# Kernel optimization log

Measured on AMD Instinct MI355X. Metric: run time of the kernel, lower is better.

Reference implementation:

```python
import jax, jax.numpy as jnp
import numpy as np

B, C, P = 16, 512, 4096


def setup_inputs() -> dict:
    key = jax.random.key(0)
    ks = jax.random.split(key, 7)
    s = 1.0 / np.sqrt(C)  # torch Conv1d default init scale
    return {
        "x": jax.random.normal(ks[0], (B, C, P), dtype=jnp.float32),
        "Wq": jax.random.uniform(ks[1], (C, C), jnp.float32, -s, s),
        "bq": jax.random.uniform(ks[2], (C,), jnp.float32, -s, s),
        "Wk": jax.random.uniform(ks[3], (C, C), jnp.float32, -s, s),
        "bk": jax.random.uniform(ks[4], (C,), jnp.float32, -s, s),
        "Wv": jax.random.uniform(ks[5], (C, C), jnp.float32, -s, s),
        "bv": jax.random.uniform(ks[6], (C,), jnp.float32, -s, s),
    }


def reference(x, Wq, bq, Wk, bk, Wv, bv):
    # 1x1 Conv1d == channel-mixing GEMM: out[b,o,p] = sum_i W[o,i] x[b,i,p] + b[o]
    q = jnp.einsum('oi,bip->bop', Wq, x) + bq[None, :, None]   # [B,C,P]
    k = jnp.einsum('oi,bip->bop', Wk, x) + bk[None, :, None]   # [B,C,P]
    v = jnp.einsum('oi,bip->bop', Wv, x) + bv[None, :, None]   # [B,C,P]
    energy = jnp.einsum('bcp,bdp->bcd', q, k)                  # [B,C,C] (unscaled)
    attn = jax.nn.softmax(energy, axis=-1)
    out = jnp.einsum('bcd,bdp->bcp', attn, v)                  # [B,C,P]
    return out
```

## Files before the change

### kernel.cpp

```cpp
#include <hip/hip_runtime.h>
#include <hip/hip_bf16.h>

#define CD 512
#define PD 4096
#define BD 16
#define CAUG 640
#define KW 576

typedef __bf16 bf16x8 __attribute__((ext_vector_type(8)));
typedef float f32x4 __attribute__((ext_vector_type(4)));
typedef unsigned short u16x8 __attribute__((ext_vector_type(8)));
typedef unsigned short u16x4 __attribute__((ext_vector_type(4)));

__device__ __forceinline__ unsigned short f2bf(float f) {
  unsigned u = __builtin_bit_cast(unsigned, f);
  u += 0x7FFFu + ((u >> 16) & 1u);
  return (unsigned short)(u >> 16);
}
__device__ __forceinline__ float bf2f(unsigned short h) {
  unsigned u = ((unsigned)h) << 16;
  return __builtin_bit_cast(float, u);
}

__global__ void convert_w2(const float* __restrict__ Wq, const float* __restrict__ bq,
                           const float* __restrict__ Wk, const float* __restrict__ bk,
                           const float* __restrict__ Wv,
                           unsigned short* __restrict__ Wqh, unsigned short* __restrict__ Wql,
                           unsigned short* __restrict__ Wkh, unsigned short* __restrict__ Wkl,
                           unsigned short* __restrict__ Wvh) {
  int i = blockIdx.x * 256 + threadIdx.x;
  if (i >= CD * KW) return;
  int o = i / KW, j = i - o * KW;
  float q = j < CD ? Wq[o * CD + j] : (j == CD ? bq[o] : 0.f);
  float k = j < CD ? Wk[o * CD + j] : (j == CD ? bk[o] : 0.f);
  unsigned short qh = f2bf(q), kh = f2bf(k);
  Wqh[i] = qh; Wql[i] = f2bf(q - bf2f(qh));
  Wkh[i] = kh; Wkl[i] = f2bf(k - bf2f(kh));
  if (j < CD) Wvh[o * CD + j] = f2bf(Wv[o * CD + j]);
}

__global__ void convert_x(const float* __restrict__ x, unsigned short* __restrict__ xsh,
                          unsigned short* __restrict__ xsl, unsigned short* __restrict__ xth) {
  int z = blockIdx.z, cy = blockIdx.y;
  int p0 = blockIdx.x * 64;
  int t = threadIdx.x;
  if (cy >= 8) {
    int row = 512 + (cy - 8) * 64 + (t >> 2);
    int cg = (t & 3) * 16;
    u16x8 h = (u16x8)0, l = (u16x8)0;
    if (row == 512)
#pragma unroll
      for (int i = 0; i < 8; ++i) h[i] = 0x3F80;
    size_t o = (size_t)z * CAUG * PD + (size_t)row * PD + p0 + cg;
    *reinterpret_cast<u16x8*>(xsh + o) = h;
    *reinterpret_cast<u16x8*>(xsh + o + 8) = h;
    *reinterpret_cast<u16x8*>(xsl + o) = l;
    *reinterpret_cast<u16x8*>(xsl + o + 8) = l;
    return;
  }
  __shared__ float tile[64][65];
  int c0 = cy * 64;
  const float* xb = x + (size_t)z * CD * PD;
  int tr = t >> 4, tc = t & 15;
#pragma unroll
  for (int j = 0; j < 4; ++j) {
    int r = tr + j * 16;
    const float* src = xb + (size_t)(c0 + r) * PD + p0 + tc * 4;
#pragma unroll
    for (int i = 0; i < 4; ++i) tile[r][tc * 4 + i] = src[i];
  }
  __syncthreads();
#pragma unroll
  for (int j = 0; j < 4; ++j) {
    int r = tr + j * 16;
    u16x4 hv, lv;
#pragma unroll
    for (int i = 0; i < 4; ++i) {
      float v = tile[r][tc * 4 + i];
      unsigned short h = f2bf(v);
      hv[i] = h; lv[i] = f2bf(v - bf2f(h));
    }
    size_t o = (size_t)z * CAUG * PD + (size_t)(c0 + r) * PD + p0 + tc * 4;
    *reinterpret_cast<u16x4*>(xsh + o) = hv;
    *reinterpret_cast<u16x4*>(xsl + o) = lv;
  }
#pragma unroll
  for (int j = 0; j < 4; ++j) {
    int pr = tr + j * 16;
    u16x4 hv;
#pragma unroll
    for (int i = 0; i < 4; ++i) hv[i] = f2bf(tile[tc * 4 + i][pr]);
    size_t o = (size_t)z * PD * CD + (size_t)(p0 + pr) * CD + c0 + tc * 4;
    *reinterpret_cast<u16x4*>(xth + o) = hv;
  }
}

enum { EPI_F32 = 0, EPI_HILO = 1, EPI_V = 2 };

template <int BM, int BN, int WM, int WN, bool SPLIT, int EPI, bool TRI>
__global__ __launch_bounds__((BM / WM) * (BN / WN) * 64) void gemm2(
    const unsigned short* __restrict__ Ahi, const unsigned short* __restrict__ Alo,
    const unsigned short* __restrict__ Bhi, const unsigned short* __restrict__ Blo,
    long long sA, long long sB, int ldA, int ldB, int K,
    float* __restrict__ Cf, unsigned short* __restrict__ Chi, unsigned short* __restrict__ Clo,
    long long sC, int ldC, const float* __restrict__ bias, int gx, int gy) {
  constexpr int BK = 64;
  constexpr int WAVES = (BM / WM) * (BN / WN);
  constexpr int NS = SPLIT ? 2 : 1;
  constexpr int MI = WM / 16, NI = WN / 16;
  constexpr int NWN = BN / WN;
  constexpr int CA = BM / 8, CB = BN / 8;
  constexpr int TOT = NS * (CA + CB);
  __shared__ unsigned short lds[NS * (BM + BN) * BK];

  int nwg = gridDim.x;
  int b = blockIdx.x;
  int q = nwg >> 3, r = nwg & 7, xcd = b & 7, pos = b >> 3;
  int wg = (xcd < r ? xcd * (q + 1) : r * (q + 1) + (xcd - r) * q) + pos;
  int bx, by, z;
  if constexpr (TRI) {
    int tri = gy * (gy + 1) / 2;
    z = wg / tri;
    int tp = wg - z * tri;
    bx = 0;
    while (tp >= gy - bx) { tp -= gy - bx; ++bx; }
    by = bx + tp;
  } else {
    by = wg % gy;
    int t2 = wg / gy;
    bx = t2 % gx;
    z = t2 / gx;
  }

  const unsigned short* pA0 = Ahi + (size_t)z * sA + (size_t)bx * BM * ldA;
  const unsigned short* pB0 = Bhi + (size_t)z * sB + (size_t)by * BN * ldB;
  const unsigned short* pA1 = SPLIT ? Alo + (size_t)z * sA + (size_t)bx * BM * ldA : pA0;
  const unsigned short* pB1 = SPLIT ? Blo + (size_t)z * sB + (size_t)by * BN * ldB : pB0;

  int tid = threadIdx.x;
  int lane = tid & 63, wid = tid >> 6;
  int wr = wid / NWN, wc = wid % NWN;
  int lr = lane & 15, kh2 = lane >> 4;

  f32x4 acc[MI][NI] = {};

  for (int k0 = 0; k0 < K; k0 += BK) {
#pragma unroll
    for (int i = 0; i < TOT / WAVES; ++i) {
      int c = wid + i * WAVES;
      const unsigned short* srcb; int ldX, lofs, rb2;
      if (c < CA)            { srcb = pA0; ldX = ldA; lofs = c * 512;                       rb2 = c * 8; }
      else if (c < NS * CA)  { srcb = pA1; ldX = ldA; lofs = BM * BK + (c - CA) * 512;      rb2 = (c - CA) * 8; }
      else if (c < NS * CA + CB) { int cc = c - NS * CA; srcb = pB0; ldX = ldB;
                                   lofs = NS * BM * BK + cc * 512;                          rb2 = cc * 8; }
      else                   { int cc = c - NS * CA - CB; srcb = pB1; ldX = ldB;
                               lofs = NS * BM * BK + BN * BK + cc * 512;                    rb2 = cc * 8; }
      int row = rb2 + (lane >> 3);
      const unsigned short* src =
          srcb + (size_t)row * ldX + k0 + (((lane & 7) ^ (row & 7)) << 3);
      __builtin_amdgcn_global_load_lds(
          (const __attribute__((address_space(1))) void*)src,
          (__attribute__((address_space(3))) void*)(lds + lofs), 16, 0, 0);
    }
    __syncthreads();

#pragma unroll
    for (int kk = 0; kk < BK / 32; ++kk) {
      bf16x8 ah[MI], al[MI], bh[NI], bl[NI];
#pragma unroll
      for (int m = 0; m < MI; ++m) {
        int row = wr * WM + m * 16 + lr;
        int so = ((((kk << 2) | kh2) ^ (row & 7)) << 3);
        ah[m] = *reinterpret_cast<const bf16x8*>(&lds[row * BK + so]);
        if constexpr (SPLIT)
          al[m] = *reinterpret_cast<const bf16x8*>(&lds[BM * BK + row * BK + so]);
      }
#pragma unroll
      for (int n = 0; n < NI; ++n) {
        int row = wc * WN + n * 16 + lr;
        int so = ((((kk << 2) | kh2) ^ (row & 7)) << 3);
        bh[n] = *reinterpret_cast<const bf16x8*>(&lds[NS * BM * BK + row * BK + so]);
        if constexpr (SPLIT)
          bl[n] = *reinterpret_cast<const bf16x8*>(&lds[NS * BM * BK + BN * BK + row * BK + so]);
      }
#pragma unroll
      for (int m = 0; m < MI; ++m)
#pragma unroll
        for (int n = 0; n < NI; ++n) {
          acc[m][n] = __builtin_amdgcn_mfma_f32_16x16x32_bf16(ah[m], bh[n], acc[m][n], 0, 0, 0);
          if constexpr (SPLIT) {
            acc[m][n] = __builtin_amdgcn_mfma_f32_16x16x32_bf16(ah[m], bl[n], acc[m][n], 0, 0, 0);
            acc[m][n] = __builtin_amdgcn_mfma_f32_16x16x32_bf16(al[m], bh[n], acc[m][n], 0, 0, 0);
          }
        }
    }
    __syncthreads();
  }

  int lg = lane >> 4;
  int rb = bx * BM + wr * WM;
  int cbase = by * BN + wc * WN;
#pragma unroll
  for (int m = 0; m < MI; ++m)
#pragma unroll
    for (int n = 0; n < NI; ++n) {
      int col = cbase + n * 16 + lr;
      float bcol = (EPI == EPI_V) ? bias[col] : 0.f;
#pragma unroll
      for (int r4 = 0; r4 < 4; ++r4) {
        int row = rb + m * 16 + lg * 4 + r4;
        size_t idx = (size_t)z * sC + (size_t)row * ldC + col;
        float v = acc[m][n][r4];
        if constexpr (EPI == EPI_F32) {
          Cf[idx] = v;
        } else if constexpr (EPI == EPI_HILO) {
          unsigned short h = f2bf(v);
          Chi[idx] = h;
          Clo[idx] = f2bf(v - bf2f(h));
        } else {
          Chi[idx] = f2bf(v + bcol);
        }
      }
    }
}

__global__ void mirror_g(unsigned short* __restrict__ Ghi, unsigned short* __restrict__ Glo) {
  __shared__ unsigned short shh[64][72], shl[64][72];
  int z = blockIdx.y;
  int pidx = blockIdx.x >> 2, sub = blockIdx.x & 3;
  int bx = 0, tp = pidx;
  while (tp >= 4 - bx) { tp -= 4 - bx; ++bx; }
  int by = bx + 1 + tp;
  int ti = bx * 2 + (sub & 1), tj = by * 2 + (sub >> 1);
  int t = threadIdx.x;
  int rr = t >> 2, cg = (t & 3) * 16;
  size_t gbase = (size_t)z * CAUG * CAUG;
  size_t so = gbase + (size_t)(ti * 64 + rr) * CAUG + tj * 64 + cg;
  *reinterpret_cast<u16x8*>(&shh[rr][cg]) = *reinterpret_cast<const u16x8*>(Ghi + so);
  *reinterpret_cast<u16x8*>(&shh[rr][cg + 8]) = *reinterpret_cast<const u16x8*>(Ghi + so + 8);
  *reinterpret_cast<u16x8*>(&shl[rr][cg]) = *reinterpret_cast<const u16x8*>(Glo + so);
  *reinterpret_cast<u16x8*>(&shl[rr][cg + 8]) = *reinterpret_cast<const u16x8*>(Glo + so + 8);
  __syncthreads();
  u16x8 oh, ol;
  size_t dst = gbase + (size_t)(tj * 64 + rr) * CAUG + ti * 64 + cg;
#pragma unroll
  for (int half = 0; half < 2; ++half) {
#pragma unroll
    for (int i = 0; i < 8; ++i) {
      oh[i] = shh[cg + half * 8 + i][rr];
      ol[i] = shl[cg + half * 8 + i][rr];
    }
    *reinterpret_cast<u16x8*>(Ghi + dst + half * 8) = oh;
    *reinterpret_cast<u16x8*>(Glo + dst + half * 8) = ol;
  }
}

__global__ void softmax_rows(const float* __restrict__ E, unsigned short* __restrict__ attn) {
  int lane = threadIdx.x & 63, wid = threadIdx.x >> 6;
  size_t row = (size_t)blockIdx.x * 4 + wid;
  const float* e = E + row * CD;
  const float4* ep = reinterpret_cast<const float4*>(e + lane * 8);
  float4 a = ep[0], bq4 = ep[1];
  float v[8] = {a.x, a.y, a.z, a.w, bq4.x, bq4.y, bq4.z, bq4.w};
  float m = v[0];
#pragma unroll
  for (int i = 1; i < 8; ++i) m = fmaxf(m, v[i]);
  for (int o = 32; o > 0; o >>= 1) m = fmaxf(m, __shfl_xor(m, o));
  float s = 0.f;
#pragma unroll
  for (int i = 0; i < 8; ++i) { v[i] = __expf(v[i] - m); s += v[i]; }
  for (int o = 32; o > 0; o >>= 1) s += __shfl_xor(s, o);
  float rinv = 1.0f / s;
  u16x4 h0, h1;
#pragma unroll
  for (int i = 0; i < 4; ++i) { h0[i] = f2bf(v[i] * rinv); h1[i] = f2bf(v[4 + i] * rinv); }
  unsigned short* op = attn + row * CD + lane * 8;
  *reinterpret_cast<u16x4*>(op) = h0;
  *reinterpret_cast<u16x4*>(op + 4) = h1;
}

extern "C" void kernel_launch(void* const* d_in, const int* in_sizes, int n_in,
                              void* d_out, int out_size, void* d_ws, size_t ws_size,
                              hipStream_t stream) {
  (void)in_sizes; (void)n_in; (void)out_size;
  const float* x  = (const float*)d_in[0];
  const float* Wq = (const float*)d_in[1];
  const float* bq = (const float*)d_in[2];
  const float* Wk = (const float*)d_in[3];
  const float* bk = (const float*)d_in[4];
  const float* Wv = (const float*)d_in[5];
  const float* bv = (const float*)d_in[6];
  float* out = (float*)d_out;

  char* base = (char*)d_ws;
  size_t off = 0;
  auto carve = [&](size_t bytes) -> char* {
    char* p = base + off;
    off += (bytes + 255) & ~(size_t)255;
    return p;
  };
  unsigned short* Wqh = (unsigned short*)carve((size_t)CD * KW * 2);
  unsigned short* Wql = (unsigned short*)carve((size_t)CD * KW * 2);
  unsigned short* Wkh = (unsigned short*)carve((size_t)CD * KW * 2);
  unsigned short* Wkl = (unsigned short*)carve((size_t)CD * KW * 2);
  unsigned short* Wvh = (unsigned short*)carve((size_t)CD * CD * 2);

  const size_t CP = (size_t)CD * PD;
  const size_t XS = (size_t)CAUG * PD;
  const size_t XT = (size_t)PD * CD;
  const size_t GG = (size_t)CAUG * CAUG;
  const size_t TT = (size_t)CD * CAUG;
  const size_t EE = (size_t)CD * CD;
  const size_t per_batch = 2 * XS * 2 + XT * 2 + 2 * GG * 2 + 2 * TT * 2 + EE * 4 + EE * 2 + XT * 2 + 2048;
  size_t rem = (ws_size > off + 4096) ? (ws_size - off - 4096) : 0;
  int nb = (int)(rem / per_batch);
  if (nb < 1) nb = 1;
  if (nb > BD) nb = BD;

  unsigned short* xsh = (unsigned short*)carve((size_t)nb * XS * 2);
  unsigned short* xsl = (unsigned short*)carve((size_t)nb * XS * 2);
  unsigned short* xth = (unsigned short*)carve((size_t)nb * XT * 2);
  unsigned short* Ghi = (unsigned short*)carve((size_t)nb * GG * 2);
  unsigned short* Glo = (unsigned short*)carve((size_t)nb * GG * 2);
  unsigned short* Thi = (unsigned short*)carve((size_t)nb * TT * 2);
  unsigned short* Tlo = (unsigned short*)carve((size_t)nb * TT * 2);
  float*          E   = (float*)carve((size_t)nb * EE * 4);
  unsigned short* att = (unsigned short*)carve((size_t)nb * EE * 2);
  unsigned short* vT  = (unsigned short*)carve((size_t)nb * XT * 2);

  convert_w2<<<dim3((CD * KW + 255) / 256), 256, 0, stream>>>(
      Wq, bq, Wk, bk, Wv, Wqh, Wql, Wkh, Wkl, Wvh);

  for (int b0 = 0; b0 < BD; b0 += nb) {
    int cb = (BD - b0 < nb) ? (BD - b0) : nb;

    convert_x<<<dim3(PD / 64, 10, cb), 256, 0, stream>>>(x + (size_t)b0 * CP, xsh, xsl, xth);

    gemm2<128, 128, 64, 32, true, EPI_HILO, true><<<15 * cb, 512, 0, stream>>>(
        xsh, xsl, xsh, xsl, (long long)XS, (long long)XS, PD, PD, PD,
        nullptr, Ghi, Glo, (long long)GG, CAUG, nullptr, 5, 5);

    mirror_g<<<dim3(40, cb), 256, 0, stream>>>(Ghi, Glo);

    gemm2<64, 64, 32, 32, true, EPI_HILO, false><<<8 * 10 * cb, 256, 0, stream>>>(
        Wqh, Wql, Ghi, Glo, 0, (long long)GG, KW, CAUG, KW,
        nullptr, Thi, Tlo, (long long)TT, CAUG, nullptr, 8, 10);

    gemm2<64, 64, 32, 32, true, EPI_F32, false><<<8 * 8 * cb, 256, 0, stream>>>(
        Thi, Tlo, Wkh, Wkl, (long long)TT, 0, CAUG, KW, KW,
        E, nullptr, nullptr, (long long)EE, CD, nullptr, 8, 8);

    softmax_rows<<<dim3(cb * CD / 4), 256, 0, stream>>>(E, att);

    gemm2<128, 128, 64, 64, false, EPI_V, false><<<32 * 4 * cb, 256, 0, stream>>>(
        xth, nullptr, Wvh, nullptr, (long long)XT, 0, CD, CD, CD,
        nullptr, vT, nullptr, (long long)XT, CD, bv, 32, 4);

    gemm2<128, 128, 64, 64, false, EPI_F32, false><<<4 * 32 * cb, 256, 0, stream>>>(
        att, nullptr, vT, nullptr, (long long)EE, (long long)XT, CD, CD, CD,
        out + (size_t)b0 * CP, nullptr, nullptr, (long long)CP, PD, nullptr, 4, 32);
  }
}
```

Baseline: 392.2 us.

## Split-K the Gram matrix GEMM with a separate reduction kernel

The triangular Gram GEMM (x·xᵀ over P=4096) runs only 15 workgroups per batch. It is now split along K into 4 slices that write fp32 partial tiles into a compact buffer, which reuses the E workspace. A new gram_reduce kernel sums the partials and writes the hi/lo bf16 split into G. The goal is more parallelism and better CU occupancy, at the cost of extra fp32 traffic and one more launch.

```diff
diff --git a/kernel.cpp b/kernel.cpp
--- a/kernel.cpp
+++ b/kernel.cpp
@@ -6,6 +6,7 @@
 #define BD 16
 #define CAUG 640
 #define KW 576
+#define GKS 4
 
 typedef __bf16 bf16x8 __attribute__((ext_vector_type(8)));
 typedef float f32x4 __attribute__((ext_vector_type(4)));
@@ -97,7 +98,7 @@
 
 enum { EPI_F32 = 0, EPI_HILO = 1, EPI_V = 2 };
 
-template <int BM, int BN, int WM, int WN, bool SPLIT, int EPI, bool TRI>
+template <int BM, int BN, int WM, int WN, bool SPLIT, int EPI, bool TRI, int SPLITK = 1>
 __global__ __launch_bounds__((BM / WM) * (BN / WN) * 64) void gemm2(
     const unsigned short* __restrict__ Ahi, const unsigned short* __restrict__ Alo,
     const unsigned short* __restrict__ Bhi, const unsigned short* __restrict__ Blo,
@@ -111,25 +112,33 @@
   constexpr int NWN = BN / WN;
   constexpr int CA = BM / 8, CB = BN / 8;
   constexpr int TOT = NS * (CA + CB);
+  constexpr bool COMPACT = TRI && (SPLITK > 1);
   __shared__ unsigned short lds[NS * (BM + BN) * BK];
 
   int nwg = gridDim.x;
   int b = blockIdx.x;
   int q = nwg >> 3, r = nwg & 7, xcd = b & 7, pos = b >> 3;
   int wg = (xcd < r ? xcd * (q + 1) : r * (q + 1) + (xcd - r) * q) + pos;
-  int bx, by, z;
+  int bx, by, z, zc, tpi = 0, kbase = 0;
   if constexpr (TRI) {
     int tri = gy * (gy + 1) / 2;
-    z = wg / tri;
-    int tp = wg - z * tri;
+    int perz = tri * SPLITK;
+    z = wg / perz;
+    int rem = wg - z * perz;
+    int ks = rem / tri;
+    tpi = rem - ks * tri;
+    int tp = tpi;
     bx = 0;
     while (tp >= gy - bx) { tp -= gy - bx; ++bx; }
     by = bx + tp;
+    kbase = ks * K;
+    zc = z * SPLITK + ks;
   } else {
     by = wg % gy;
     int t2 = wg / gy;
     bx = t2 % gx;
     z = t2 / gx;
+    zc = z;
   }
 
   const unsigned short* pA0 = Ahi + (size_t)z * sA + (size_t)bx * BM * ldA;
@@ -144,17 +153,17 @@
 
   f32x4 acc[MI][NI] = {};
 
-  for (int k0 = 0; k0 < K; k0 += BK) {
+  for (int k0 = kbase; k0 < kbase + K; k0 += BK) {
 #pragma unroll
     for (int i = 0; i < TOT / WAVES; ++i) {
       int c = wid + i * WAVES;
       const unsigned short* srcb; int ldX, lofs, rb2;
-      if (c < CA)            { srcb = pA0; ldX = ldA; lofs = c * 512;                       rb2 = c * 8; }
-      else if (c < NS * CA)  { srcb = pA1; ldX = ldA; lofs = BM * BK + (c - CA) * 512;      rb2 = (c - CA) * 8; }
+      if (c < CA)            { srcb = pA0; ldX = ldA; lofs = c * 512;                  rb2 = c * 8; }
+      else if (c < NS * CA)  { srcb = pA1; ldX = ldA; lofs = BM * BK + (c - CA) * 512; rb2 = (c - CA) * 8; }
       else if (c < NS * CA + CB) { int cc = c - NS * CA; srcb = pB0; ldX = ldB;
-                                   lofs = NS * BM * BK + cc * 512;                          rb2 = cc * 8; }
+                                   lofs = NS * BM * BK + cc * 512;                     rb2 = cc * 8; }
       else                   { int cc = c - NS * CA - CB; srcb = pB1; ldX = ldB;
-                               lofs = NS * BM * BK + BN * BK + cc * 512;                    rb2 = cc * 8; }
+                               lofs = NS * BM * BK + BN * BK + cc * 512;               rb2 = cc * 8; }
       int row = rb2 + (lane >> 3);
       const unsigned short* src =
           srcb + (size_t)row * ldX + k0 + (((lane & 7) ^ (row & 7)) << 3);
@@ -198,30 +207,65 @@
   }
 
   int lg = lane >> 4;
-  int rb = bx * BM + wr * WM;
-  int cbase = by * BN + wc * WN;
 #pragma unroll
   for (int m = 0; m < MI; ++m)
 #pragma unroll
     for (int n = 0; n < NI; ++n) {
-      int col = cbase + n * 16 + lr;
-      float bcol = (EPI == EPI_V) ? bias[col] : 0.f;
+      int lcol = wc * WN + n * 16 + lr;
+      float bcol = (EPI == EPI_V) ? bias[by * BN + lcol] : 0.f;
 #pragma unroll
       for (int r4 = 0; r4 < 4; ++r4) {
-        int row = rb + m * 16 + lg * 4 + r4;
-        size_t idx = (size_t)z * sC + (size_t)row * ldC + col;
+        int lrow = wr * WM + m * 16 + lg * 4 + r4;
         float v = acc[m][n][r4];
-        if constexpr (EPI == EPI_F32) {
+        if constexpr (COMPACT) {
+          size_t idx = (size_t)zc * sC + (size_t)tpi * (BM * BN) + (size_t)lrow * BN + lcol;
           Cf[idx] = v;
-        } else if constexpr (EPI == EPI_HILO) {
-          unsigned short h = f2bf(v);
-          Chi[idx] = h;
-          Clo[idx] = f2bf(v - bf2f(h));
         } else {
-          Chi[idx] = f2bf(v + bcol);
+          size_t idx = (size_t)zc * sC + (size_t)(bx * BM + lrow) * ldC + (by * BN + lcol);
+          if constexpr (EPI == EPI_F32) {
+            Cf[idx] = v;
+          } else if constexpr (EPI == EPI_HILO) {
+            unsigned short h = f2bf(v);
+            Chi[idx] = h;
+            Clo[idx] = f2bf(v - bf2f(h));
+          } else {
+            Chi[idx] = f2bf(v + bcol);
+          }
         }
       }
     }
+}
+
+template <int KS>
+__global__ void gram_reduce(const float* __restrict__ Gp,
+                            unsigned short* __restrict__ Ghi, unsigned short* __restrict__ Glo) {
+  int z = blockIdx.y;
+  int tp = blockIdx.x;
+  int b2 = tp, bx = 0;
+  while (b2 >= 5 - bx) { b2 -= 5 - bx; ++bx; }
+  int by = bx + b2;
+  int t = threadIdx.x;
+  const float* base = Gp + ((size_t)z * KS * 15 + tp) * (128 * 128);
+  size_t gb = (size_t)z * CAUG * CAUG;
+#pragma unroll
+  for (int it = 0; it < 16; ++it) {
+    int lrow = it * 8 + (t >> 5);
+    int lc = (t & 31) * 4;
+    f32x4 s = *reinterpret_cast<const f32x4*>(base + (size_t)lrow * 128 + lc);
+#pragma unroll
+    for (int ks = 1; ks < KS; ++ks)
+      s += *reinterpret_cast<const f32x4*>(base + (size_t)ks * 15 * 128 * 128 +
+                                           (size_t)lrow * 128 + lc);
+    u16x4 h, l;
+#pragma unroll
+    for (int i = 0; i < 4; ++i) {
+      unsigned short hh = f2bf(s[i]);
+      h[i] = hh; l[i] = f2bf(s[i] - bf2f(hh));
+    }
+    size_t o = gb + (size_t)(bx * 128 + lrow) * CAUG + by * 128 + lc;
+    *reinterpret_cast<u16x4*>(Ghi + o) = h;
+    *reinterpret_cast<u16x4*>(Glo + o) = l;
+  }
 }
 
 __global__ void mirror_g(unsigned short* __restrict__ Ghi, unsigned short* __restrict__ Glo) {
@@ -328,6 +372,8 @@
   unsigned short* att = (unsigned short*)carve((size_t)nb * EE * 2);
   unsigned short* vT  = (unsigned short*)carve((size_t)nb * XT * 2);
 
+  float* Gpart = E;
+
   convert_w2<<<dim3((CD * KW + 255) / 256), 256, 0, stream>>>(
       Wq, bq, Wk, bk, Wv, Wqh, Wql, Wkh, Wkl, Wvh);
 
@@ -336,9 +382,11 @@
 
     convert_x<<<dim3(PD / 64, 10, cb), 256, 0, stream>>>(x + (size_t)b0 * CP, xsh, xsl, xth);
 
-    gemm2<128, 128, 64, 32, true, EPI_HILO, true><<<15 * cb, 512, 0, stream>>>(
-        xsh, xsl, xsh, xsl, (long long)XS, (long long)XS, PD, PD, PD,
-        nullptr, Ghi, Glo, (long long)GG, CAUG, nullptr, 5, 5);
+    gemm2<128, 128, 64, 32, true, EPI_F32, true, GKS><<<15 * GKS * cb, 512, 0, stream>>>(
+        xsh, xsl, xsh, xsl, (long long)XS, (long long)XS, PD, PD, PD / GKS,
+        Gpart, nullptr, nullptr, (long long)15 * 128 * 128, 128, nullptr, 5, 5);
+
+    gram_reduce<GKS><<<dim3(15, cb), 256, 0, stream>>>(Gpart, Ghi, Glo);
 
     mirror_g<<<dim3(40, cb), 256, 0, stream>>>(Ghi, Glo);
 
```

After: 352.6 us. -10.1%, faster.
